# Kernel optimization log

Measured on AMD Instinct MI355X. Metric: run time of the kernel, lower is better.

The kernel has to match this reference:

```python
import jax, jax.numpy as jnp
import numpy as np

B, T, OBS = 16, 256, 128
W0 = 256          # widths = [256, 256], num_hidden = 1
HID = 256         # rnn_hidden_dim
CTX = 64
A = 64            # action_dim
RANK = 4
HN_H = 128        # hypernet hidden
DELTA_SCALE = 0.05
LV_MIN, LV_MAX = -6.0, 4.0


def setup_inputs() -> dict:
    key = jax.random.key(0)
    ks = jax.random.split(key, 32)
    s = 0.05
    def w(k, shape):
        return jax.random.normal(k, shape, dtype=jnp.float32) * s
    HN_OUT = HID * RANK + RANK * A + A  # 1344
    return {
        "obs_seq": jax.random.normal(ks[0], (B, T, OBS), dtype=jnp.float32),
        "h0": jnp.zeros((1, B, HID), dtype=jnp.float32),
        # encoder MLP (torch Linear convention: W is [out, in])
        "W_in": w(ks[1], (W0, OBS)),   "b_in": w(ks[2], (W0,)),
        "W_h1": w(ks[3], (W0, W0)),    "b_h1": w(ks[4], (W0,)),
        # GRU (gate order r, z, n as in torch)
        "gru_Wih": w(ks[5], (3 * HID, W0)),  "gru_Whh": w(ks[6], (3 * HID, HID)),
        "gru_bih": w(ks[7], (3 * HID,)),     "gru_bhh": w(ks[8], (3 * HID,)),
        # context heads
        "W_mu": w(ks[9], (CTX, HID)),  "b_mu": w(ks[10], (CTX,)),
        "W_lv": w(ks[11], (CTX, HID)), "b_lv": w(ks[12], (CTX,)),
        # scalar gate params
        "gate_w": jnp.float32(1.0), "gate_b": jnp.float32(0.0),
        # base policy head
        "W_pol": w(ks[13], (A, HID)), "b_pol": w(ks[14], (A,)),
        # hypernet MLP: ctx -> 128 -> 128 -> HN_OUT
        "hn_W1": w(ks[15], (HN_H, CTX)),  "hn_b1": w(ks[16], (HN_H,)),
        "hn_W2": w(ks[17], (HN_H, HN_H)), "hn_b2": w(ks[18], (HN_H,)),
        "hn_W3": w(ks[19], (HN_OUT, HN_H)), "hn_b3": w(ks[20], (HN_OUT,)),
    }


def _gru(x_seq, h0, Wih, Whh, bih, bhh):
    """Batch-first GRU. x_seq: [B,T,D], h0: [B,H] -> (feats [B,T,H], hT [B,H])."""
    # precompute input-side gate pre-activations: [T, B, 3H]
    xg = jnp.einsum("btd,gd->tbg", x_seq, Wih) + bih

    def step(h, xg_t):
        hg = h @ Whh.T + bhh                       # [B, 3H]
        xr, xz, xn = jnp.split(xg_t, 3, axis=-1)
        hr, hz, hn = jnp.split(hg, 3, axis=-1)
        r = jax.nn.sigmoid(xr + hr)
        z = jax.nn.sigmoid(xz + hz)
        n = jnp.tanh(xn + r * hn)
        h_new = (1.0 - z) * n + z * h
        return h_new, h_new

    hT, feats = jax.lax.scan(step, h0, xg)
    return jnp.transpose(feats, (1, 0, 2)), hT      # [B,T,H], [B,H]


def reference(obs_seq, h0, W_in, b_in, W_h1, b_h1,
              gru_Wih, gru_Whh, gru_bih, gru_bhh,
              W_mu, b_mu, W_lv, b_lv, gate_w, gate_b,
              W_pol, b_pol, hn_W1, hn_b1, hn_W2, hn_b2, hn_W3, hn_b3):
    # ---- encoder MLP ----
    x = jax.nn.relu(obs_seq @ W_in.T + b_in)
    x = jax.nn.relu(x @ W_h1.T + b_h1)             # [B,T,W0]

    # ---- GRU ----
    feats, hT = _gru(x, h0[0], gru_Wih, gru_Whh, gru_bih, gru_bhh)  # [B,T,H]
    hn_state = hT[None]                            # [1,B,H]

    # ---- context heads + uncertainty gate ----
    ctx_mu = feats @ W_mu.T + b_mu                 # [B,T,CTX]
    ctx_lv = jnp.clip(feats @ W_lv.T + b_lv, LV_MIN, LV_MAX)
    mean_lv = jnp.mean(ctx_lv, axis=-1, keepdims=True)      # [B,T,1]
    gate = jax.nn.sigmoid(gate_w * (-mean_lv) + gate_b)     # [B,T,1]

    # ---- low-rank hypernet deltas ----
    h1 = jax.nn.relu(ctx_mu @ hn_W1.T + hn_b1)
    h2 = jax.nn.relu(h1 @ hn_W2.T + hn_b2)
    deltas = (h2 @ hn_W3.T + hn_b3) * DELTA_SCALE  # [B,T,H*r + r*A + A]
    w_end = HID * RANK
    a_end = w_end + RANK * A
    Bn, Tn = obs_seq.shape[0], obs_seq.shape[1]
    wf = deltas[..., :w_end].reshape(Bn, Tn, HID, RANK)     # [B,T,H,r]
    af = deltas[..., w_end:a_end].reshape(Bn, Tn, RANK, A)  # [B,T,r,A]
    db = deltas[..., a_end:]                                # [B,T,A]

    delta_w = jnp.einsum("bthr,btra->btha", wf, af)         # [B,T,H,A] (large)
    base_w = W_pol.T[None, None]                            # [1,1,H,A]
    eff_w = base_w + gate[..., None] * delta_w
    eff_b = b_pol[None, None] + gate * db
    logits = jnp.einsum("bth,btha->bta", feats, eff_w) + eff_b
    return logits, hn_state
```

## Files before the change

kernel.cpp:

```cpp
#include <hip/hip_runtime.h>
#include <cstddef>

#define BB 16
#define TT 256
#define OBSD 128
#define W0D 256
#define HID 256
#define CTX 64
#define NA 64
#define HNH 128
#define HNOUT 1344
#define MROWS 4096

__device__ __forceinline__ float sigm(float x) { return 1.f / (1.f + __expf(-x)); }
__device__ __forceinline__ float tanh_f(float x) { return 1.f - 2.f / (__expf(2.f * x) + 1.f); }

__global__ __launch_bounds__(256) void gemm_bt(
    const float* __restrict__ A, const float* __restrict__ Bw,
    const float* __restrict__ bias, float* __restrict__ C,
    int M, int N, int K, int act, float scale)
{
    __shared__ float As[16][132];
    __shared__ float Bs[16][68];
    const int tid = threadIdx.x;
    const int m0 = blockIdx.x * 128, n0 = blockIdx.y * 64;
    const int tx = tid & 15, ty = tid >> 4;
    float acc[8][4] = {};
    for (int k0 = 0; k0 < K; k0 += 16) {
#pragma unroll
        for (int l = 0; l < 2; ++l) {
            int v = tid + l * 256;
            int row = v >> 2, kc = (v & 3) << 2;
            float4 a4 = *(const float4*)(A + (size_t)(m0 + row) * K + k0 + kc);
            As[kc + 0][row] = a4.x; As[kc + 1][row] = a4.y;
            As[kc + 2][row] = a4.z; As[kc + 3][row] = a4.w;
        }
        {
            int row = tid >> 2, kc = (tid & 3) << 2;
            float4 b4 = *(const float4*)(Bw + (size_t)(n0 + row) * K + k0 + kc);
            Bs[kc + 0][row] = b4.x; Bs[kc + 1][row] = b4.y;
            Bs[kc + 2][row] = b4.z; Bs[kc + 3][row] = b4.w;
        }
        __syncthreads();
#pragma unroll
        for (int k = 0; k < 16; ++k) {
            float4 a0 = *(const float4*)&As[k][ty * 8];
            float4 a1 = *(const float4*)&As[k][ty * 8 + 4];
            float4 b0 = *(const float4*)&Bs[k][tx * 4];
            float a[8] = {a0.x, a0.y, a0.z, a0.w, a1.x, a1.y, a1.z, a1.w};
            float b[4] = {b0.x, b0.y, b0.z, b0.w};
#pragma unroll
            for (int i = 0; i < 8; ++i)
#pragma unroll
                for (int jj = 0; jj < 4; ++jj)
                    acc[i][jj] = fmaf(a[i], b[jj], acc[i][jj]);
        }
        __syncthreads();
    }
    const float4 bia = *(const float4*)(bias + n0 + tx * 4);
    const float bb[4] = {bia.x, bia.y, bia.z, bia.w};
#pragma unroll
    for (int i = 0; i < 8; ++i) {
        int m = m0 + ty * 8 + i;
        float4 o;
        float* op = &o.x;
#pragma unroll
        for (int jj = 0; jj < 4; ++jj) {
            float v = acc[i][jj] + bb[jj];
            if (act) v = fmaxf(v, 0.f);
            op[jj] = v * scale;
        }
        *(float4*)(C + (size_t)m * N + n0 + tx * 4) = o;
    }
}

typedef _Float16 h2v __attribute__((ext_vector_type(2)));

#if defined(__has_builtin)
#if __has_builtin(__builtin_amdgcn_fdot2)
#define HAVE_FDOT2 1
#endif
#endif

__device__ __forceinline__ float dot2acc(h2v a, h2v b, float c) {
#ifdef HAVE_FDOT2
    return __builtin_amdgcn_fdot2(a, b, c, false);
#else
    return c + (float)a[0] * (float)b[0] + (float)a[1] * (float)b[1];
#endif
}

__global__ __launch_bounds__(512, 2) void gru_kernel(
    const float* __restrict__ XG, const float* __restrict__ Whh,
    const float* __restrict__ bhh, const float* __restrict__ h0,
    float* __restrict__ FE, float* __restrict__ HT)
{
    __shared__ __align__(16) _Float16 hbuf[HID];
    __shared__ float part[3][HID];
    const int b = blockIdx.x;
    const int tid = threadIdx.x;
    const int j = tid & 255, ks = tid >> 8;
    h2v w[3][64];
#pragma unroll
    for (int r = 0; r < 3; ++r) {
        const float* wr = Whh + (size_t)(r * HID + j) * HID + ks * 128;
#pragma unroll
        for (int i = 0; i < 64; ++i) {
            float2 f = *(const float2*)(wr + 2 * i);
            h2v t; t[0] = (_Float16)f.x; t[1] = (_Float16)f.y;
            w[r][i] = t;
        }
    }
    const float br = bhh[j], bz = bhh[HID + j], bn = bhh[2 * HID + j];
    float hj = 0.f;
    if (ks == 0) {
        hj = h0[b * HID + j];
        hbuf[j] = (_Float16)hj;
    }
    __syncthreads();
    const float* xg = XG + (size_t)b * TT * 768;
    for (int t = 0; t < TT; ++t) {
        float xr = 0.f, xz = 0.f, xn = 0.f;
        if (ks == 0) {
            const float* p = xg + (size_t)t * 768 + j;
            xr = p[0]; xz = p[256]; xn = p[512];
        }
        float pr = 0.f, pz = 0.f, pn = 0.f;
        const h2v* hp = (const h2v*)hbuf + ks * 64;
#pragma unroll
        for (int i = 0; i < 64; ++i) {
            h2v hh = hp[i];
            pr = dot2acc(w[0][i], hh, pr);
            pz = dot2acc(w[1][i], hh, pz);
            pn = dot2acc(w[2][i], hh, pn);
        }
        if (ks) { part[0][j] = pr; part[1][j] = pz; part[2][j] = pn; }
        __syncthreads();
        if (ks == 0) {
            float hr = pr + part[0][j] + br;
            float hz = pz + part[1][j] + bz;
            float hn = pn + part[2][j] + bn;
            float r = sigm(xr + hr);
            float z = sigm(xz + hz);
            float n = tanh_f(xn + r * hn);
            hj = (1.f - z) * n + z * hj;
            hbuf[j] = (_Float16)hj;
            FE[((size_t)b * TT + t) * HID + j] = hj;
        }
        __syncthreads();
    }
    if (ks == 0) HT[b * HID + j] = hj;
}

__global__ __launch_bounds__(256) void mid_kernel(
    const float* __restrict__ FE,
    const float* __restrict__ W_mu, const float* __restrict__ b_mu,
    const float* __restrict__ W_lv, const float* __restrict__ b_lv,
    const float* __restrict__ gw_p, const float* __restrict__ gb_p,
    const float* __restrict__ W1, const float* __restrict__ b1,
    const float* __restrict__ W2, const float* __restrict__ b2,
    float* __restrict__ GATE, float* __restrict__ H2out)
{
    __shared__ float fT[256][20];
    __shared__ float muT[64][20];
    __shared__ float h1T[128][20];
    __shared__ float lvb[16][68];
    const int tid = threadIdx.x;
    const int r0 = blockIdx.x * 16;
#pragma unroll
    for (int l = 0; l < 4; ++l) {
        int v = tid + l * 256;
        int t = v >> 6, kc = (v & 63) << 2;
        float4 f = *(const float4*)(FE + (size_t)(r0 + t) * HID + kc);
        fT[kc + 0][t] = f.x; fT[kc + 1][t] = f.y;
        fT[kc + 2][t] = f.z; fT[kc + 3][t] = f.w;
    }
    __syncthreads();
    const int c = tid & 127, tg = tid >> 7;
    {
        const float* wrow = (c < 64) ? (W_mu + (size_t)c * HID)
                                     : (W_lv + (size_t)(c - 64) * HID);
        float acc[8] = {};
        for (int k = 0; k < 256; k += 4) {
            float4 wv = *(const float4*)(wrow + k);
#pragma unroll
            for (int e = 0; e < 4; ++e) {
                float wsc = (&wv.x)[e];
                float4 fa = *(const float4*)&fT[k + e][tg * 8];
                float4 fb = *(const float4*)&fT[k + e][tg * 8 + 4];
                acc[0] = fmaf(wsc, fa.x, acc[0]); acc[1] = fmaf(wsc, fa.y, acc[1]);
                acc[2] = fmaf(wsc, fa.z, acc[2]); acc[3] = fmaf(wsc, fa.w, acc[3]);
                acc[4] = fmaf(wsc, fb.x, acc[4]); acc[5] = fmaf(wsc, fb.y, acc[5]);
                acc[6] = fmaf(wsc, fb.z, acc[6]); acc[7] = fmaf(wsc, fb.w, acc[7]);
            }
        }
        float bb2 = (c < 64) ? b_mu[c] : b_lv[c - 64];
#pragma unroll
        for (int i2 = 0; i2 < 8; ++i2) {
            int t = tg * 8 + i2;
            float v = acc[i2] + bb2;
            if (c < 64) muT[c][t] = v;
            else        lvb[t][c - 64] = fminf(fmaxf(v, -6.f), 4.f);
        }
    }
    __syncthreads();
    if (tid < 16) {
        float s = 0.f;
        for (int i2 = 0; i2 < 64; ++i2) s += lvb[tid][i2];
        float mean = s * (1.f / 64.f);
        GATE[r0 + tid] = sigm(gw_p[0] * (-mean) + gb_p[0]);
    }
    {
        const float* wrow = W1 + (size_t)c * CTX;
        float acc[8] = {};
        for (int k = 0; k < 64; k += 4) {
            float4 wv = *(const float4*)(wrow + k);
#pragma unroll
            for (int e = 0; e < 4; ++e) {
                float wsc = (&wv.x)[e];
                float4 fa = *(const float4*)&muT[k + e][tg * 8];
                float4 fb = *(const float4*)&muT[k + e][tg * 8 + 4];
                acc[0] = fmaf(wsc, fa.x, acc[0]); acc[1] = fmaf(wsc, fa.y, acc[1]);
                acc[2] = fmaf(wsc, fa.z, acc[2]); acc[3] = fmaf(wsc, fa.w, acc[3]);
                acc[4] = fmaf(wsc, fb.x, acc[4]); acc[5] = fmaf(wsc, fb.y, acc[5]);
                acc[6] = fmaf(wsc, fb.z, acc[6]); acc[7] = fmaf(wsc, fb.w, acc[7]);
            }
        }
        float bb2 = b1[c];
#pragma unroll
        for (int i2 = 0; i2 < 8; ++i2) {
            int t = tg * 8 + i2;
            h1T[c][t] = fmaxf(acc[i2] + bb2, 0.f);
        }
    }
    __syncthreads();
    {
        const float* wrow = W2 + (size_t)c * HNH;
        float acc[8] = {};
        for (int k = 0; k < 128; k += 4) {
            float4 wv = *(const float4*)(wrow + k);
#pragma unroll
            for (int e = 0; e < 4; ++e) {
                float wsc = (&wv.x)[e];
                float4 fa = *(const float4*)&h1T[k + e][tg * 8];
                float4 fb = *(const float4*)&h1T[k + e][tg * 8 + 4];
                acc[0] = fmaf(wsc, fa.x, acc[0]); acc[1] = fmaf(wsc, fa.y, acc[1]);
                acc[2] = fmaf(wsc, fa.z, acc[2]); acc[3] = fmaf(wsc, fa.w, acc[3]);
                acc[4] = fmaf(wsc, fb.x, acc[4]); acc[5] = fmaf(wsc, fb.y, acc[5]);
                acc[6] = fmaf(wsc, fb.z, acc[6]); acc[7] = fmaf(wsc, fb.w, acc[7]);
            }
        }
        float bb2 = b2[c];
#pragma unroll
        for (int i2 = 0; i2 < 8; ++i2) {
            int t = tg * 8 + i2;
            H2out[(size_t)(r0 + t) * HNH + c] = fmaxf(acc[i2] + bb2, 0.f);
        }
    }
}

__global__ __launch_bounds__(256) void final_kernel(
    const float* __restrict__ FE, const float* __restrict__ DL,
    const float* __restrict__ GATE, const float* __restrict__ W_pol,
    const float* __restrict__ b_pol, float* __restrict__ OUT)
{
    __shared__ float fs[4][256];
    __shared__ float dsb[4][HNOUT];
    __shared__ float sr[4][4];
    __shared__ float gg[4];
    const int tid = threadIdx.x;
    const int r0 = blockIdx.x * 4;
    {
        int t = tid >> 6, kc = (tid & 63) << 2;
        *(float4*)&fs[t][kc] = *(const float4*)(FE + (size_t)(r0 + t) * HID + kc);
    }
    for (int v = tid; v < 1344; v += 256) {
        int t = v / 336, q = v - t * 336;
        ((float4*)&dsb[t][0])[q] = ((const float4*)(DL + (size_t)(r0 + t) * HNOUT))[q];
    }
    if (tid < 4) gg[tid] = GATE[r0 + tid];
    __syncthreads();
    {
        const int t = tid >> 6, lane = tid & 63;
        float p0 = 0, p1 = 0, p2 = 0, p3 = 0;
#pragma unroll
        for (int hh = 0; hh < 4; ++hh) {
            int h = lane + hh * 64;
            float f = fs[t][h];
            float4 d4 = *(const float4*)&dsb[t][4 * h];
            p0 = fmaf(f, d4.x, p0); p1 = fmaf(f, d4.y, p1);
            p2 = fmaf(f, d4.z, p2); p3 = fmaf(f, d4.w, p3);
        }
#pragma unroll
        for (int off = 32; off >= 1; off >>= 1) {
            p0 += __shfl_down(p0, off);
            p1 += __shfl_down(p1, off);
            p2 += __shfl_down(p2, off);
            p3 += __shfl_down(p3, off);
        }
        if (lane == 0) { sr[t][0] = p0; sr[t][1] = p1; sr[t][2] = p2; sr[t][3] = p3; }
    }
    __syncthreads();
    {
        const int t = tid >> 6, a = tid & 63;
        const float* wrow = W_pol + (size_t)a * HID;
        float acc = 0.f;
        for (int k = 0; k < 256; k += 4) {
            float4 wv = *(const float4*)(wrow + k);
            float4 fv = *(const float4*)&fs[t][k];
            acc = fmaf(wv.x, fv.x, acc); acc = fmaf(wv.y, fv.y, acc);
            acc = fmaf(wv.z, fv.z, acc); acc = fmaf(wv.w, fv.w, acc);
        }
        float la = sr[t][0] * dsb[t][1024 + a] + sr[t][1] * dsb[t][1088 + a]
                 + sr[t][2] * dsb[t][1152 + a] + sr[t][3] * dsb[t][1216 + a]
                 + dsb[t][1280 + a];
        OUT[(size_t)(r0 + t) * NA + a] = acc + b_pol[a] + gg[t] * la;
    }
}

extern "C" void kernel_launch(void* const* d_in, const int* in_sizes, int n_in,
                              void* d_out, int out_size, void* d_ws, size_t ws_size,
                              hipStream_t stream) {
    const float* obs   = (const float*)d_in[0];
    const float* h0    = (const float*)d_in[1];
    const float* W_in  = (const float*)d_in[2];
    const float* b_in  = (const float*)d_in[3];
    const float* W_h1  = (const float*)d_in[4];
    const float* b_h1  = (const float*)d_in[5];
    const float* Wih   = (const float*)d_in[6];
    const float* Whh   = (const float*)d_in[7];
    const float* bih   = (const float*)d_in[8];
    const float* bhh   = (const float*)d_in[9];
    const float* W_mu  = (const float*)d_in[10];
    const float* b_mu  = (const float*)d_in[11];
    const float* W_lv  = (const float*)d_in[12];
    const float* b_lv  = (const float*)d_in[13];
    const float* gate_w= (const float*)d_in[14];
    const float* gate_b= (const float*)d_in[15];
    const float* W_pol = (const float*)d_in[16];
    const float* b_pol = (const float*)d_in[17];
    const float* hn_W1 = (const float*)d_in[18];
    const float* hn_b1 = (const float*)d_in[19];
    const float* hn_W2 = (const float*)d_in[20];
    const float* hn_b2 = (const float*)d_in[21];
    const float* hn_W3 = (const float*)d_in[22];
    const float* hn_b3 = (const float*)d_in[23];

    float* ws = (float*)d_ws;
    float* X1 = ws;
    float* X2 = X1 + 1048576;
    float* XG = X2 + 1048576;
    float* FE = XG + 3145728;
    float* GA = FE + 1048576;
    float* H2 = GA + 4096;
    float* DL = H2 + 524288;
    (void)ws_size; (void)n_in; (void)in_sizes; (void)out_size;

    float* logits = (float*)d_out;
    float* hn_out = logits + (size_t)BB * TT * NA;

    gemm_bt<<<dim3(32, 4), 256, 0, stream>>>(obs, W_in, b_in, X1, MROWS, 256, 128, 1, 1.f);
    gemm_bt<<<dim3(32, 4), 256, 0, stream>>>(X1, W_h1, b_h1, X2, MROWS, 256, 256, 1, 1.f);
    gemm_bt<<<dim3(32, 12), 256, 0, stream>>>(X2, Wih, bih, XG, MROWS, 768, 256, 0, 1.f);
    gru_kernel<<<16, 512, 0, stream>>>(XG, Whh, bhh, h0, FE, hn_out);
    mid_kernel<<<256, 256, 0, stream>>>(FE, W_mu, b_mu, W_lv, b_lv, gate_w, gate_b,
                                        hn_W1, hn_b1, hn_W2, hn_b2, GA, H2);
    gemm_bt<<<dim3(32, 21), 256, 0, stream>>>(H2, hn_W3, hn_b3, DL, MROWS, HNOUT, 128, 0, 0.05f);
    final_kernel<<<1024, 256, 0, stream>>>(FE, DL, GA, W_pol, b_pol, logits);
}
```

Baseline: 576.3 us.

## Run GRU recurrence matvec on MFMA with double-buffered hidden state

Replaces the fdot2-based per-thread GRU recurrent matvec with MFMA 16x16x32 f16 instructions. Each wave holds a 32-column slice of all three gate weight matrices in registers. The hidden state is double-buffered in shared memory, which cuts the per-step synchronisation from two barriers to one and removes the cross-half partial-sum exchange. Only row 0 of the 16-row MFMA A operand carries useful data, so most of the matrix throughput is spent on padding. The gain is meant to come from shorter instruction latency on the serial critical path.

```diff
diff --git a/kernel.cpp b/kernel.cpp
--- a/kernel.cpp
+++ b/kernel.cpp
@@ -74,82 +74,87 @@
     }
 }
 
-typedef _Float16 h2v __attribute__((ext_vector_type(2)));
-
-#if defined(__has_builtin)
-#if __has_builtin(__builtin_amdgcn_fdot2)
-#define HAVE_FDOT2 1
-#endif
-#endif
-
-__device__ __forceinline__ float dot2acc(h2v a, h2v b, float c) {
-#ifdef HAVE_FDOT2
-    return __builtin_amdgcn_fdot2(a, b, c, false);
-#else
-    return c + (float)a[0] * (float)b[0] + (float)a[1] * (float)b[1];
-#endif
-}
-
-__global__ __launch_bounds__(512, 2) void gru_kernel(
+typedef _Float16 f16x8 __attribute__((ext_vector_type(8)));
+typedef float f32x4 __attribute__((ext_vector_type(4)));
+
+__global__ __launch_bounds__(512) void gru_mfma_kernel(
     const float* __restrict__ XG, const float* __restrict__ Whh,
     const float* __restrict__ bhh, const float* __restrict__ h0,
     float* __restrict__ FE, float* __restrict__ HT)
 {
-    __shared__ __align__(16) _Float16 hbuf[HID];
-    __shared__ float part[3][HID];
+    __shared__ __align__(16) _Float16 hbuf[2][16 * 264];
     const int b = blockIdx.x;
     const int tid = threadIdx.x;
-    const int j = tid & 255, ks = tid >> 8;
-    h2v w[3][64];
-#pragma unroll
-    for (int r = 0; r < 3; ++r) {
-        const float* wr = Whh + (size_t)(r * HID + j) * HID + ks * 128;
-#pragma unroll
-        for (int i = 0; i < 64; ++i) {
-            float2 f = *(const float2*)(wr + 2 * i);
-            h2v t; t[0] = (_Float16)f.x; t[1] = (_Float16)f.y;
-            w[r][i] = t;
-        }
-    }
-    const float br = bhh[j], bz = bhh[HID + j], bn = bhh[2 * HID + j];
-    float hj = 0.f;
-    if (ks == 0) {
-        hj = h0[b * HID + j];
-        hbuf[j] = (_Float16)hj;
-    }
-    __syncthreads();
-    const float* xg = XG + (size_t)b * TT * 768;
+    const int wv = tid >> 6;
+    const int l  = tid & 63;
+    const int c  = l & 15;
+    const int q  = l >> 4;
+
+    f16x8 wreg[6][8];
+#pragma unroll
+    for (int ti = 0; ti < 6; ++ti) {
+        const int g = ti >> 1;
+        const int j = 32 * wv + (ti & 1) * 16 + c;
+        const float* row = Whh + (size_t)(g * 256 + j) * 256 + q * 8;
+#pragma unroll
+        for (int ks = 0; ks < 8; ++ks) {
+            float4 f0 = *(const float4*)(row + ks * 32);
+            float4 f1 = *(const float4*)(row + ks * 32 + 4);
+            f16x8 v;
+            v[0] = (_Float16)f0.x; v[1] = (_Float16)f0.y;
+            v[2] = (_Float16)f0.z; v[3] = (_Float16)f0.w;
+            v[4] = (_Float16)f1.x; v[5] = (_Float16)f1.y;
+            v[6] = (_Float16)f1.z; v[7] = (_Float16)f1.w;
+            wreg[ti][ks] = v;
+        }
+    }
+    const int j1 = 32 * wv + c, j2 = j1 + 16;
+    const float br1 = bhh[j1], bz1 = bhh[256 + j1], bn1 = bhh[512 + j1];
+    const float br2 = bhh[j2], bz2 = bhh[256 + j2], bn2 = bhh[512 + j2];
+    float h1o = 0.f, h2o = 0.f;
+    if (l < 16) {
+        h1o = h0[b * 256 + j1]; h2o = h0[b * 256 + j2];
+        hbuf[0][j1] = (_Float16)h1o; hbuf[0][j2] = (_Float16)h2o;
+    }
+    __syncthreads();
+    const float* xgp = XG + (size_t)b * TT * 768;
+    float* fep = FE + (size_t)b * TT * HID;
     for (int t = 0; t < TT; ++t) {
-        float xr = 0.f, xz = 0.f, xn = 0.f;
-        if (ks == 0) {
-            const float* p = xg + (size_t)t * 768 + j;
-            xr = p[0]; xz = p[256]; xn = p[512];
-        }
-        float pr = 0.f, pz = 0.f, pn = 0.f;
-        const h2v* hp = (const h2v*)hbuf + ks * 64;
-#pragma unroll
-        for (int i = 0; i < 64; ++i) {
-            h2v hh = hp[i];
-            pr = dot2acc(w[0][i], hh, pr);
-            pz = dot2acc(w[1][i], hh, pz);
-            pn = dot2acc(w[2][i], hh, pn);
-        }
-        if (ks) { part[0][j] = pr; part[1][j] = pz; part[2][j] = pn; }
+        float xr1, xz1, xn1, xr2, xz2, xn2;
+        if (l < 16) {
+            xr1 = xgp[j1]; xz1 = xgp[256 + j1]; xn1 = xgp[512 + j1];
+            xr2 = xgp[j2]; xz2 = xgp[256 + j2]; xn2 = xgp[512 + j2];
+        }
+        f32x4 a0 = {0.f, 0.f, 0.f, 0.f}, a1 = a0, a2 = a0,
+              a3 = a0, a4 = a0, a5 = a0;
+        const _Float16* hb = hbuf[t & 1] + c * 264 + q * 8;
+#pragma unroll
+        for (int ks = 0; ks < 8; ++ks) {
+            f16x8 af = *(const f16x8*)(hb + ks * 32);
+            a0 = __builtin_amdgcn_mfma_f32_16x16x32_f16(af, wreg[0][ks], a0, 0, 0, 0);
+            a1 = __builtin_amdgcn_mfma_f32_16x16x32_f16(af, wreg[1][ks], a1, 0, 0, 0);
+            a2 = __builtin_amdgcn_mfma_f32_16x16x32_f16(af, wreg[2][ks], a2, 0, 0, 0);
+            a3 = __builtin_amdgcn_mfma_f32_16x16x32_f16(af, wreg[3][ks], a3, 0, 0, 0);
+            a4 = __builtin_amdgcn_mfma_f32_16x16x32_f16(af, wreg[4][ks], a4, 0, 0, 0);
+            a5 = __builtin_amdgcn_mfma_f32_16x16x32_f16(af, wreg[5][ks], a5, 0, 0, 0);
+        }
+        if (l < 16) {
+            float r1 = sigm(xr1 + a0[0] + br1);
+            float z1 = sigm(xz1 + a2[0] + bz1);
+            float n1 = tanh_f(xn1 + r1 * (a4[0] + bn1));
+            h1o = (1.f - z1) * n1 + z1 * h1o;
+            float r2 = sigm(xr2 + a1[0] + br2);
+            float z2 = sigm(xz2 + a3[0] + bz2);
+            float n2 = tanh_f(xn2 + r2 * (a5[0] + bn2));
+            h2o = (1.f - z2) * n2 + z2 * h2o;
+            _Float16* nb = hbuf[(t + 1) & 1];
+            nb[j1] = (_Float16)h1o; nb[j2] = (_Float16)h2o;
+            fep[j1] = h1o; fep[j2] = h2o;
+        }
+        xgp += 768; fep += HID;
         __syncthreads();
-        if (ks == 0) {
-            float hr = pr + part[0][j] + br;
-            float hz = pz + part[1][j] + bz;
-            float hn = pn + part[2][j] + bn;
-            float r = sigm(xr + hr);
-            float z = sigm(xz + hz);
-            float n = tanh_f(xn + r * hn);
-            hj = (1.f - z) * n + z * hj;
-            hbuf[j] = (_Float16)hj;
-            FE[((size_t)b * TT + t) * HID + j] = hj;
-        }
-        __syncthreads();
-    }
-    if (ks == 0) HT[b * HID + j] = hj;
+    }
+    if (l < 16) { HT[b * HID + j1] = h1o; HT[b * HID + j2] = h2o; }
 }
 
 __global__ __launch_bounds__(256) void mid_kernel(
@@ -275,8 +280,8 @@
         *(float4*)&fs[t][kc] = *(const float4*)(FE + (size_t)(r0 + t) * HID + kc);
     }
     for (int v = tid; v < 1344; v += 256) {
-        int t = v / 336, q = v - t * 336;
-        ((float4*)&dsb[t][0])[q] = ((const float4*)(DL + (size_t)(r0 + t) * HNOUT))[q];
+        int t = v / 336, qq = v - t * 336;
+        ((float4*)&dsb[t][0])[qq] = ((const float4*)(DL + (size_t)(r0 + t) * HNOUT))[qq];
     }
     if (tid < 4) gg[tid] = GATE[r0 + tid];
     __syncthreads();
@@ -362,7 +367,7 @@
     gemm_bt<<<dim3(32, 4), 256, 0, stream>>>(obs, W_in, b_in, X1, MROWS, 256, 128, 1, 1.f);
     gemm_bt<<<dim3(32, 4), 256, 0, stream>>>(X1, W_h1, b_h1, X2, MROWS, 256, 256, 1, 1.f);
     gemm_bt<<<dim3(32, 12), 256, 0, stream>>>(X2, Wih, bih, XG, MROWS, 768, 256, 0, 1.f);
-    gru_kernel<<<16, 512, 0, stream>>>(XG, Whh, bhh, h0, FE, hn_out);
+    gru_mfma_kernel<<<16, 512, 0, stream>>>(XG, Whh, bhh, h0, FE, hn_out);
     mid_kernel<<<256, 256, 0, stream>>>(FE, W_mu, b_mu, W_lv, b_lv, gate_w, gate_b,
                                         hn_W1, hn_b1, hn_W2, hn_b2, GA, H2);
     gemm_bt<<<dim3(32, 21), 256, 0, stream>>>(H2, hn_W3, hn_b3, DL, MROWS, HNOUT, 128, 0, 0.05f);
```

After: 579.2 us. Within noise of the previous version (+0.5%).
